# Kernel optimization log

Hardware: AMD Instinct MI355X
Metric: run time of the kernel (lower is better)

The kernel has to match this reference:

```python
import jax, jax.numpy as jnp
import numpy as np

D_MODEL = 512
EXPAND = 2
D_INNER = D_MODEL * EXPAND  # 1024
D_STATE = 64
D_CONV = 4
DT_BASE = 0.1
MAX_STEPS = 10
THRESH = 1e-4
DAMPING = 0.5
B_SZ, L = 1, 256


def setup_inputs() -> dict:
    key = jax.random.key(0)
    ks = jax.random.split(key, 12)
    rn = lambda k, shape, s=0.02: jax.random.normal(k, shape, jnp.float32) * s
    x = jax.random.normal(ks[0], (B_SZ, L, D_MODEL), jnp.float32)
    # in_proj: Linear(d_model -> 2*d_inner, bias=False); stored (in, out)
    W_in = rn(ks[1], (D_MODEL, 2 * D_INNER))
    # depthwise causal conv1d, kernel (d_inner, 1, d_conv) + bias
    conv_w = rn(ks[2], (D_INNER, 1, D_CONV), 0.2)
    conv_b = rn(ks[3], (D_INNER,), 0.02)
    # SSM kernel params (A_log initialized exactly as in the module)
    A_log = jnp.log(jnp.broadcast_to(jnp.arange(1, D_STATE + 1, dtype=jnp.float32), (D_INNER, D_STATE)))
    W_B = rn(ks[4], (D_INNER, D_STATE))
    W_C = rn(ks[5], (D_INNER, D_STATE))
    D = jnp.ones((D_INNER,), jnp.float32)
    dt_w1 = rn(ks[6], (D_INNER, D_INNER // 4))
    dt_b1 = jnp.zeros((D_INNER // 4,), jnp.float32)
    dt_w2 = rn(ks[7], (D_INNER // 4, D_INNER))
    dt_b2 = jnp.zeros((D_INNER,), jnp.float32)
    W_out = rn(ks[8], (D_INNER, D_MODEL))
    ln_in_g = jnp.ones((D_MODEL,), jnp.float32)
    ln_in_b = jnp.zeros((D_MODEL,), jnp.float32)
    ln_out_g = jnp.ones((D_MODEL,), jnp.float32)
    ln_out_b = jnp.zeros((D_MODEL,), jnp.float32)
    return dict(x=x, W_in=W_in, conv_w=conv_w, conv_b=conv_b, A_log=A_log, W_B=W_B, W_C=W_C, D=D,
                dt_w1=dt_w1, dt_b1=dt_b1, dt_w2=dt_w2, dt_b2=dt_b2, W_out=W_out,
                ln_in_g=ln_in_g, ln_in_b=ln_in_b, ln_out_g=ln_out_g, ln_out_b=ln_out_b)


def _ln(x, g, b, eps=1e-5):
    m = jnp.mean(x, axis=-1, keepdims=True)
    v = jnp.mean((x - m) ** 2, axis=-1, keepdims=True)
    return (x - m) / jnp.sqrt(v + eps) * g + b


def _forward(x, W_in, conv_w, conv_b, A_log, W_B, W_C, D, dt_w1, dt_b1, dt_w2, dt_b2, W_out,
             ln_in_g, ln_in_b, ln_out_g, ln_out_b):
    residual = x
    xn = _ln(x, ln_in_g, ln_in_b)
    xz = xn @ W_in                                  # (b, l, 2*d_inner)
    x_inner, z = jnp.split(xz, 2, axis=-1)
    # depthwise causal conv (pad d_conv-1 on the left == pad both sides then take [:L])
    xc = jnp.transpose(x_inner, (0, 2, 1))          # (b, d, l)
    xc = jax.lax.conv_general_dilated(xc, conv_w, window_strides=(1,),
                                      padding=[(D_CONV - 1, 0)],
                                      feature_group_count=D_INNER)
    xc = xc + conv_b[None, :, None]
    x_inner = jax.nn.silu(jnp.transpose(xc, (0, 2, 1)))  # (b, l, d_inner)

    # --- kernel quantities (loop-invariant: depend only on x_inner) ---
    A = -jnp.exp(A_log)                             # (d, n)
    Bm = x_inner @ W_B                              # (b, l, n)
    Cm = x_inner @ W_C                              # (b, l, n)
    dt = jax.nn.gelu(x_inner @ dt_w1 + dt_b1, approximate=False) @ dt_w2 + dt_b2
    dt = jax.nn.softplus(dt) * DT_BASE              # (b, l, d)
    A_bar = jnp.exp(jnp.einsum('bld,dn->bldn', dt, A))          # (b, l, d, n)
    Bx = (dt * x_inner)[..., None] * Bm[:, :, None, :]           # B_bar * x, (b, l, d, n)

    # --- fixed-point evolution with convergence-gated freeze (== early break) ---
    h = jnp.zeros_like(A_bar)
    y_h = h  # h_new that produces the output y
    converged = jnp.array(False)
    h_diff = jnp.float32(0.0)
    for _ in range(MAX_STEPS):
        h_new = A_bar * h + Bx
        dh = h_new - h
        diff = jnp.mean(jnp.sqrt(jnp.sum(dh * dh, axis=(-2, -1))))  # mean Frobenius norm over (b,l)
        y_h = jnp.where(converged, y_h, h_new)
        h_diff = jnp.where(converged, h_diff, diff)
        converged = converged | (diff < THRESH)
        # damping update skipped after break (converged)
        h = jnp.where(converged, h, DAMPING * h_new + (1.0 - DAMPING) * h)

    y = jnp.einsum('bldn,bln->bld', y_h, Cm) + D * x_inner
    y = y * jax.nn.silu(z)
    out = _ln(y @ W_out, ln_out_g, ln_out_b) + residual
    return out


def reference(x, W_in, conv_w, conv_b, A_log, W_B, W_C, D, dt_w1, dt_b1, dt_w2, dt_b2, W_out,
              ln_in_g, ln_in_b, ln_out_g, ln_out_b):
    return _forward(x, W_in, conv_w, conv_b, A_log, W_B, W_C, D, dt_w1, dt_b1, dt_w2, dt_b2,
                    W_out, ln_in_g, ln_in_b, ln_out_g, ln_out_b)
```

## Files before the change

kernel.cpp:

```cpp
#include <hip/hip_runtime.h>
#include <cmath>

#define L 256
#define DMODEL 512
#define DINNER 1024
#define DSTATE 64
#define NSTEPS 10

#define XZ_OFF 0
#define XI_OFF 1048576
#define BCT_OFF 1310720
#define DTB_OFF 2097152
#define ACC_OFF 3145728
#define YOP_OFF 3155968

__device__ __forceinline__ float gelu_f(float x) {
  return 0.5f * x * (1.0f + erff(x * 0.70710678118654752f));
}

__device__ __forceinline__ void mm_accum(const float (*As)[68],
                                         const float (*Bs)[64],
                                         float acc[4][4], int ty, int tx) {
#pragma unroll
  for (int kk = 0; kk < 32; ++kk) {
    const float4 av = *(const float4*)&As[kk][ty * 4];
    const float4 bv = *(const float4*)&Bs[kk][tx * 4];
    const float* ap = (const float*)&av;
    const float* bp = (const float*)&bv;
#pragma unroll
    for (int i = 0; i < 4; ++i)
#pragma unroll
      for (int j = 0; j < 4; ++j) acc[i][j] = fmaf(ap[i], bp[j], acc[i][j]);
  }
}

__device__ __forceinline__ void store_tile(float acc[4][4], float* C, int ldc,
                                           int m0, int nc, int ty, int tx) {
#pragma unroll
  for (int i = 0; i < 4; ++i)
    *(float4*)&C[(size_t)(m0 + ty * 4 + i) * ldc + nc + tx * 4] =
        *(float4*)&acc[i][0];
}

__global__ __launch_bounds__(256, 2) void k_inproj(
    const float* __restrict__ x, const float* __restrict__ g,
    const float* __restrict__ b, const float* __restrict__ W_in,
    float* __restrict__ xz) {
  __shared__ __align__(16) float As[32][68];
  __shared__ __align__(16) float Bs[32][64];
  __shared__ float pS[64][4], pQ[64][4];
  __shared__ float mrow[64], rrow[64];
  const int tid = threadIdx.x;
  const int ty = tid >> 4, tx = tid & 15;
  const int m0 = blockIdx.y * 64, n0 = blockIdx.x * 64;
  const int k0 = blockIdx.z * 256;
  {
    const int row = tid >> 2, part = tid & 3;
    const float* rp = &x[(size_t)(m0 + row) * DMODEL + part * 128];
    float s = 0.0f, q = 0.0f;
#pragma unroll
    for (int i = 0; i < 32; ++i) {
      const float4 v = *(const float4*)&rp[i * 4];
      s += v.x + v.y + v.z + v.w;
      q += v.x * v.x + v.y * v.y + v.z * v.z + v.w * v.w;
    }
    pS[row][part] = s;
    pQ[row][part] = q;
  }
  __syncthreads();
  if (tid < 64) {
    const float S = pS[tid][0] + pS[tid][1] + pS[tid][2] + pS[tid][3];
    const float Q = pQ[tid][0] + pQ[tid][1] + pQ[tid][2] + pQ[tid][3];
    const float m = S * (1.0f / DMODEL);
    const float v = Q * (1.0f / DMODEL) - m * m;
    mrow[tid] = m;
    rrow[tid] = rsqrtf(v + 1e-5f);
  }
  __syncthreads();
  float acc[4][4] = {};
  for (int t = 0; t < 8; ++t) {
    const int kb = k0 + t * 32;
#pragma unroll
    for (int i = 0; i < 2; ++i) {
      const int idx = tid + i * 256;
      const int r = idx >> 3, ck = (idx & 7) * 4;
      const float4 v = *(const float4*)&x[(size_t)(m0 + r) * DMODEL + kb + ck];
      const float* vp = (const float*)&v;
      const float m = mrow[r], rs = rrow[r];
#pragma unroll
      for (int j = 0; j < 4; ++j)
        As[ck + j][r] = (vp[j] - m) * rs * g[kb + ck + j] + b[kb + ck + j];
    }
#pragma unroll
    for (int i = 0; i < 2; ++i) {
      const int idx = tid + i * 256;
      const int r = idx >> 4, c = (idx & 15) * 4;
      *(float4*)&Bs[r][c] = *(const float4*)&W_in[(size_t)(kb + r) * 2048 + n0 + c];
    }
    __syncthreads();
    mm_accum(As, Bs, acc, ty, tx);
    __syncthreads();
  }
  store_tile(acc, xz + (size_t)blockIdx.z * 524288, 2048, m0, n0, ty, tx);
}

__global__ __launch_bounds__(256, 2) void k_bct(
    const float* __restrict__ xz, const float* __restrict__ cw,
    const float* __restrict__ cb, const float* __restrict__ W_B,
    const float* __restrict__ W_C, const float* __restrict__ W1,
    float* __restrict__ bctp, float* __restrict__ xi) {
  __shared__ __align__(16) float As[32][68];
  __shared__ __align__(16) float Bs[32][64];
  const int tid = threadIdx.x;
  const int ty = tid >> 4, tx = tid & 15;
  const int nt = blockIdx.x;
  const int m0 = blockIdx.y * 64, k0 = blockIdx.z * 128;
  const float* Bp;
  int ldb, nb;
  if (nt == 0) { Bp = W_B; ldb = 64; nb = 0; }
  else if (nt == 1) { Bp = W_C; ldb = 64; nb = 0; }
  else { Bp = W1; ldb = 256; nb = (nt - 2) * 64; }
  float acc[4][4] = {};
  for (int t = 0; t < 4; ++t) {
    const int kb = k0 + t * 32;
#pragma unroll
    for (int i = 0; i < 2; ++i) {
      const int idx = tid + i * 256;
      const int r = idx >> 3, ck = (idx & 7) * 4;
      const int l = m0 + r, d0 = kb + ck;
      float v[4];
      {
        const float4 cbv = *(const float4*)&cb[d0];
        v[0] = cbv.x; v[1] = cbv.y; v[2] = cbv.z; v[3] = cbv.w;
      }
      float4 wq[4];
#pragma unroll
      for (int j = 0; j < 4; ++j) wq[j] = *(const float4*)&cw[(d0 + j) * 4];
      const float* w0 = (const float*)&wq[0];
      const float* w1 = (const float*)&wq[1];
      const float* w2 = (const float*)&wq[2];
      const float* w3 = (const float*)&wq[3];
#pragma unroll
      for (int j = 0; j < 4; ++j) {
        const int ll = l - 3 + j;
        if (ll >= 0) {
          const float4 u0 = *(const float4*)&xz[(size_t)ll * 2048 + d0];
          const float4 u1 = *(const float4*)&xz[524288 + (size_t)ll * 2048 + d0];
          v[0] = fmaf(w0[j], u0.x + u1.x, v[0]);
          v[1] = fmaf(w1[j], u0.y + u1.y, v[1]);
          v[2] = fmaf(w2[j], u0.z + u1.z, v[2]);
          v[3] = fmaf(w3[j], u0.w + u1.w, v[3]);
        }
      }
#pragma unroll
      for (int j = 0; j < 4; ++j) v[j] = v[j] / (1.0f + expf(-v[j]));
      if (nt == 0)
        *(float4*)&xi[(size_t)l * DINNER + d0] = *(float4*)&v[0];
#pragma unroll
      for (int j = 0; j < 4; ++j) As[ck + j][r] = v[j];
    }
#pragma unroll
    for (int i = 0; i < 2; ++i) {
      const int idx = tid + i * 256;
      const int r = idx >> 4, c = (idx & 15) * 4;
      *(float4*)&Bs[r][c] = *(const float4*)&Bp[(size_t)(kb + r) * ldb + nb + c];
    }
    __syncthreads();
    mm_accum(As, Bs, acc, ty, tx);
    __syncthreads();
  }
  store_tile(acc, bctp + (size_t)blockIdx.z * 98304, 384, m0, nt * 64, ty, tx);
}

__global__ __launch_bounds__(256, 2) void k_dt2(
    const float* __restrict__ bctp, const float* __restrict__ dt_b1,
    const float* __restrict__ dt_w2, float* __restrict__ dtbp) {
  __shared__ __align__(16) float As[32][68];
  __shared__ __align__(16) float Bs[32][64];
  const int tid = threadIdx.x;
  const int ty = tid >> 4, tx = tid & 15;
  const int m0 = blockIdx.y * 64, n0 = blockIdx.x * 64;
  const int k0 = blockIdx.z * 64;
  float acc[4][4] = {};
  for (int t = 0; t < 2; ++t) {
    const int kb = k0 + t * 32;
#pragma unroll
    for (int i = 0; i < 2; ++i) {
      const int idx = tid + i * 256;
      const int r = idx >> 3, ck = (idx & 7) * 4;
      const float4 bv = *(const float4*)&dt_b1[kb + ck];
      float v[4] = {bv.x, bv.y, bv.z, bv.w};
#pragma unroll
      for (int s = 0; s < 8; ++s) {
        const float4 u =
            *(const float4*)&bctp[s * 98304 + (size_t)(m0 + r) * 384 + 128 + kb + ck];
        v[0] += u.x; v[1] += u.y; v[2] += u.z; v[3] += u.w;
      }
#pragma unroll
      for (int j = 0; j < 4; ++j) As[ck + j][r] = gelu_f(v[j]);
    }
#pragma unroll
    for (int i = 0; i < 2; ++i) {
      const int idx = tid + i * 256;
      const int r = idx >> 4, c = (idx & 15) * 4;
      *(float4*)&Bs[r][c] =
          *(const float4*)&dt_w2[(size_t)(kb + r) * 1024 + n0 + c];
    }
    __syncthreads();
    mm_accum(As, Bs, acc, ty, tx);
    __syncthreads();
  }
  store_tile(acc, dtbp + (size_t)blockIdx.z * 262144, 1024, m0, n0, ty, tx);
}

__global__ __launch_bounds__(256, 2) void k_pass1(
    const float* __restrict__ dtbp, const float* __restrict__ dt_b2,
    const float* __restrict__ xi, const float* __restrict__ bctp,
    float* __restrict__ accLp) {
  const int bx = blockIdx.x, l = blockIdx.y, tid = threadIdx.x;
  const int d = bx * 256 + tid;
  __shared__ float B2[DSTATE];
  __shared__ float sred[4][NSTEPS];
  if (tid < DSTATE) {
    float b = 0.0f;
#pragma unroll
    for (int s = 0; s < 8; ++s) b += bctp[s * 98304 + l * 384 + tid];
    B2[tid] = b * b;
  }
  __syncthreads();
  float dr = dt_b2[d];
#pragma unroll
  for (int s = 0; s < 4; ++s) dr += dtbp[s * 262144 + l * DINNER + d];
  const float sp = (dr > 20.0f) ? dr : log1pf(expf(dr));
  const float dtv = 0.1f * sp;
  const float xv = xi[l * DINNER + d];
  float w0 = dtv * xv;
  w0 *= w0;
  const float q = expf(-dtv);
  float acc[NSTEPS] = {};
  float aa = 1.0f;
  for (int n = 0; n < DSTATE; ++n) {
    aa *= q;
    const float r = fmaf(0.5f, aa, 0.5f);
    const float s2 = r * r;
    float p = w0 * B2[n];
#pragma unroll
    for (int k = 0; k < NSTEPS; ++k) {
      acc[k] += p;
      p *= s2;
    }
  }
#pragma unroll
  for (int k = 0; k < NSTEPS; ++k) {
    float v = acc[k];
#pragma unroll
    for (int off = 32; off; off >>= 1) v += __shfl_down(v, off);
    if ((tid & 63) == 0) sred[tid >> 6][k] = v;
  }
  __syncthreads();
  if (tid < NSTEPS)
    accLp[bx * (L * NSTEPS) + l * NSTEPS + tid] =
        sred[0][tid] + sred[1][tid] + sred[2][tid] + sred[3][tid];
}

__global__ __launch_bounds__(256, 2) void k_pass2(
    const float* __restrict__ dtbp, const float* __restrict__ dt_b2,
    const float* __restrict__ xi_in, const float* __restrict__ bctp,
    const float* __restrict__ xz, const float* __restrict__ Dv,
    const float* __restrict__ accLp, float* __restrict__ y) {
  const int bx = blockIdx.x, l = blockIdx.y, tid = threadIdx.x;
  const int d = bx * 256 + tid;
  __shared__ float sred[4];
  __shared__ float diffs[NSTEPS];
  __shared__ float P[DSTATE];
  __shared__ int Ksh;
#pragma unroll
  for (int k = 0; k < NSTEPS; ++k) {
    float v = 0.0f;
#pragma unroll
    for (int s = 0; s < 4; ++s) v += accLp[s * 2560 + tid * NSTEPS + k];
    v = sqrtf(v);
#pragma unroll
    for (int off = 32; off; off >>= 1) v += __shfl_down(v, off);
    if ((tid & 63) == 0) sred[tid >> 6] = v;
    __syncthreads();
    if (tid == 0)
      diffs[k] = (sred[0] + sred[1] + sred[2] + sred[3]) * (1.0f / L);
    __syncthreads();
  }
  if (tid == 0) {
    int K = NSTEPS;
    for (int k = 0; k < NSTEPS; ++k) {
      if (diffs[k] < 1e-4f) { K = k + 1; break; }
    }
    Ksh = K;
  }
  if (tid < DSTATE) {
    float bm = 0.0f, cm = 0.0f;
#pragma unroll
    for (int s = 0; s < 8; ++s) {
      bm += bctp[s * 98304 + l * 384 + tid];
      cm += bctp[s * 98304 + l * 384 + 64 + tid];
    }
    P[tid] = bm * cm;
  }
  __syncthreads();
  const int K = Ksh;
  float dr = dt_b2[d];
#pragma unroll
  for (int s = 0; s < 4; ++s) dr += dtbp[s * 262144 + l * DINNER + d];
  const float sp = (dr > 20.0f) ? dr : log1pf(expf(dr));
  const float dtv = 0.1f * sp;
  const float xv = xi_in[l * DINNER + d];
  const float dtx = dtv * xv;
  const float q = expf(-dtv);
  float aa = 1.0f, s = 0.0f;
  for (int n = 0; n < DSTATE; ++n) {
    aa *= q;
    const float r = fmaf(0.5f, aa, 0.5f);
    float c = 0.0f;
    for (int k = 1; k < K; ++k) c = fmaf(r, c, 0.5f);
    const float hn = fmaf(aa, c, 1.0f);
    s = fmaf(hn, P[n], s);
  }
  float yv = fmaf(dtx, s, Dv[d] * xv);
  const float zv = xz[l * 2048 + 1024 + d] + xz[524288 + l * 2048 + 1024 + d];
  yv *= zv / (1.0f + expf(-zv));
  y[l * DINNER + d] = yv;
}

__global__ __launch_bounds__(256, 2) void k_outproj(
    const float* __restrict__ yv, const float* __restrict__ W_out,
    float* __restrict__ yop) {
  __shared__ __align__(16) float As[32][68];
  __shared__ __align__(16) float Bs[32][64];
  const int tid = threadIdx.x;
  const int ty = tid >> 4, tx = tid & 15;
  const int m0 = blockIdx.y * 64, n0 = blockIdx.x * 64;
  const int k0 = blockIdx.z * 128;
  float acc[4][4] = {};
  for (int t = 0; t < 4; ++t) {
    const int kb = k0 + t * 32;
#pragma unroll
    for (int i = 0; i < 2; ++i) {
      const int idx = tid + i * 256;
      const int r = idx >> 3, ck = (idx & 7) * 4;
      const float4 v = *(const float4*)&yv[(size_t)(m0 + r) * DINNER + kb + ck];
      const float* vp = (const float*)&v;
#pragma unroll
      for (int j = 0; j < 4; ++j) As[ck + j][r] = vp[j];
    }
#pragma unroll
    for (int i = 0; i < 2; ++i) {
      const int idx = tid + i * 256;
      const int r = idx >> 4, c = (idx & 15) * 4;
      *(float4*)&Bs[r][c] =
          *(const float4*)&W_out[(size_t)(kb + r) * DMODEL + n0 + c];
    }
    __syncthreads();
    mm_accum(As, Bs, acc, ty, tx);
    __syncthreads();
  }
  store_tile(acc, yop + (size_t)blockIdx.z * 131072, DMODEL, m0, n0, ty, tx);
}

__global__ __launch_bounds__(256, 2) void k_ln2(
    const float* __restrict__ yop, const float* __restrict__ g,
    const float* __restrict__ b, const float* __restrict__ resid,
    float* __restrict__ out) {
  const int l = blockIdx.x, tid = threadIdx.x;
  float x0 = 0.0f, x1 = 0.0f;
#pragma unroll
  for (int s = 0; s < 8; ++s) {
    x0 += yop[s * 131072 + l * DMODEL + tid];
    x1 += yop[s * 131072 + l * DMODEL + tid + 256];
  }
  float sm = x0 + x1, q = x0 * x0 + x1 * x1;
#pragma unroll
  for (int off = 32; off; off >>= 1) {
    sm += __shfl_down(sm, off);
    q += __shfl_down(q, off);
  }
  __shared__ float sw[4], qw[4];
  __shared__ float mS, rS;
  if ((tid & 63) == 0) { sw[tid >> 6] = sm; qw[tid >> 6] = q; }
  __syncthreads();
  if (tid == 0) {
    float S = sw[0] + sw[1] + sw[2] + sw[3];
    float Q = qw[0] + qw[1] + qw[2] + qw[3];
    float m = S * (1.0f / DMODEL);
    float v = Q * (1.0f / DMODEL) - m * m;
    mS = m;
    rS = rsqrtf(v + 1e-5f);
  }
  __syncthreads();
  const float m = mS, r = rS;
  out[l * DMODEL + tid] =
      (x0 - m) * r * g[tid] + b[tid] + resid[l * DMODEL + tid];
  out[l * DMODEL + tid + 256] =
      (x1 - m) * r * g[tid + 256] + b[tid + 256] + resid[l * DMODEL + tid + 256];
}

extern "C" void kernel_launch(void* const* d_in, const int* in_sizes, int n_in,
                              void* d_out, int out_size, void* d_ws,
                              size_t ws_size, hipStream_t stream) {
  const float* x = (const float*)d_in[0];
  const float* W_in = (const float*)d_in[1];
  const float* conv_w = (const float*)d_in[2];
  const float* conv_b = (const float*)d_in[3];
  const float* W_B = (const float*)d_in[5];
  const float* W_C = (const float*)d_in[6];
  const float* Dv = (const float*)d_in[7];
  const float* dt_w1 = (const float*)d_in[8];
  const float* dt_b1 = (const float*)d_in[9];
  const float* dt_w2 = (const float*)d_in[10];
  const float* dt_b2 = (const float*)d_in[11];
  const float* W_out = (const float*)d_in[12];
  const float* ln_in_g = (const float*)d_in[13];
  const float* ln_in_b = (const float*)d_in[14];
  const float* ln_out_g = (const float*)d_in[15];
  const float* ln_out_b = (const float*)d_in[16];
  float* out = (float*)d_out;

  float* ws = (float*)d_ws;
  float* xz = ws + XZ_OFF;
  float* xi = ws + XI_OFF;
  float* bctp = ws + BCT_OFF;
  float* dtbp = ws + DTB_OFF;
  float* accLp = ws + ACC_OFF;
  float* yop = ws + YOP_OFF;

  k_inproj<<<dim3(32, 4, 2), 256, 0, stream>>>(x, ln_in_g, ln_in_b, W_in, xz);
  k_bct<<<dim3(6, 4, 8), 256, 0, stream>>>(xz, conv_w, conv_b, W_B, W_C,
                                           dt_w1, bctp, xi);
  k_dt2<<<dim3(16, 4, 4), 256, 0, stream>>>(bctp, dt_b1, dt_w2, dtbp);
  k_pass1<<<dim3(4, L), 256, 0, stream>>>(dtbp, dt_b2, xi, bctp, accLp);
  k_pass2<<<dim3(4, L), 256, 0, stream>>>(dtbp, dt_b2, xi, bctp, xz, Dv,
                                          accLp, xi);
  k_outproj<<<dim3(8, 4, 8), 256, 0, stream>>>(xi, W_out, yop);
  k_ln2<<<L, 256, 0, stream>>>(yop, ln_out_g, ln_out_b, x, out);
}
```

Before: 214.7 us.

## Split prologue work out of GEMMs into dedicated elementwise kernels

Moves LayerNorm, the causal conv plus SiLU, and the z gate out of the GEMM A-tile loaders into separate elementwise kernels (k_ln1, k_convz, k_prep). All projections then run through one generic k_gemm with different split-K factors. Precomputed B^2, B*C and the gelu'd dt hidden layer are shared by pass1 and pass2 instead of being recomputed per block. This removes redundant per-tile recomputation of conv, norm and gelu inside the GEMMs, at the cost of three extra kernel launches and extra global-memory round trips.

```diff
diff --git a/kernel.cpp b/kernel.cpp
--- a/kernel.cpp
+++ b/kernel.cpp
@@ -7,12 +7,17 @@
 #define DSTATE 64
 #define NSTEPS 10
 
-#define XZ_OFF 0
-#define XI_OFF 1048576
-#define BCT_OFF 1310720
-#define DTB_OFF 2097152
-#define ACC_OFF 3145728
-#define YOP_OFF 3155968
+#define XN_OFF 0
+#define XZ_OFF 131072
+#define XI_OFF 2228224
+#define ZS_OFF 2490368
+#define BCT_OFF 2752512
+#define T1S_OFF 3538944
+#define B2_OFF 3604480
+#define P_OFF 3620864
+#define DTB_OFF 3637248
+#define ACC_OFF 4161536
+#define YOP_OFF 4171776
 
 __device__ __forceinline__ float gelu_f(float x) {
   return 0.5f * x * (1.0f + erff(x * 0.70710678118654752f));
@@ -42,73 +47,101 @@
         *(float4*)&acc[i][0];
 }
 
-__global__ __launch_bounds__(256, 2) void k_inproj(
-    const float* __restrict__ x, const float* __restrict__ g,
-    const float* __restrict__ b, const float* __restrict__ W_in,
-    float* __restrict__ xz) {
+__global__ __launch_bounds__(256) void k_ln1(
+    const float* __restrict__ in, const float* __restrict__ g,
+    const float* __restrict__ b, float* __restrict__ out) {
+  const int l = blockIdx.x, tid = threadIdx.x;
+  const float x0 = in[l * DMODEL + tid];
+  const float x1 = in[l * DMODEL + tid + 256];
+  float sm = x0 + x1, q = x0 * x0 + x1 * x1;
+#pragma unroll
+  for (int off = 32; off; off >>= 1) {
+    sm += __shfl_down(sm, off);
+    q += __shfl_down(q, off);
+  }
+  __shared__ float sw[4], qw[4];
+  __shared__ float mS, rS;
+  if ((tid & 63) == 0) { sw[tid >> 6] = sm; qw[tid >> 6] = q; }
+  __syncthreads();
+  if (tid == 0) {
+    float S = sw[0] + sw[1] + sw[2] + sw[3];
+    float Q = qw[0] + qw[1] + qw[2] + qw[3];
+    float m = S * (1.0f / DMODEL);
+    float v = Q * (1.0f / DMODEL) - m * m;
+    mS = m;
+    rS = rsqrtf(v + 1e-5f);
+  }
+  __syncthreads();
+  out[l * DMODEL + tid] = (x0 - mS) * rS * g[tid] + b[tid];
+  out[l * DMODEL + tid + 256] = (x1 - mS) * rS * g[tid + 256] + b[tid + 256];
+}
+
+__global__ __launch_bounds__(256, 2) void k_gemm(
+    const float* __restrict__ A, int lda, const float* __restrict__ B, int ldb,
+    float* __restrict__ C, int ldc, int cslice, int kchunk) {
   __shared__ __align__(16) float As[32][68];
   __shared__ __align__(16) float Bs[32][64];
-  __shared__ float pS[64][4], pQ[64][4];
-  __shared__ float mrow[64], rrow[64];
   const int tid = threadIdx.x;
   const int ty = tid >> 4, tx = tid & 15;
   const int m0 = blockIdx.y * 64, n0 = blockIdx.x * 64;
-  const int k0 = blockIdx.z * 256;
-  {
-    const int row = tid >> 2, part = tid & 3;
-    const float* rp = &x[(size_t)(m0 + row) * DMODEL + part * 128];
-    float s = 0.0f, q = 0.0f;
-#pragma unroll
-    for (int i = 0; i < 32; ++i) {
-      const float4 v = *(const float4*)&rp[i * 4];
-      s += v.x + v.y + v.z + v.w;
-      q += v.x * v.x + v.y * v.y + v.z * v.z + v.w * v.w;
-    }
-    pS[row][part] = s;
-    pQ[row][part] = q;
-  }
-  __syncthreads();
-  if (tid < 64) {
-    const float S = pS[tid][0] + pS[tid][1] + pS[tid][2] + pS[tid][3];
-    const float Q = pQ[tid][0] + pQ[tid][1] + pQ[tid][2] + pQ[tid][3];
-    const float m = S * (1.0f / DMODEL);
-    const float v = Q * (1.0f / DMODEL) - m * m;
-    mrow[tid] = m;
-    rrow[tid] = rsqrtf(v + 1e-5f);
-  }
-  __syncthreads();
+  const int k0 = blockIdx.z * kchunk;
+  const int ktiles = kchunk >> 5;
   float acc[4][4] = {};
-  for (int t = 0; t < 8; ++t) {
+  for (int t = 0; t < ktiles; ++t) {
     const int kb = k0 + t * 32;
 #pragma unroll
     for (int i = 0; i < 2; ++i) {
       const int idx = tid + i * 256;
       const int r = idx >> 3, ck = (idx & 7) * 4;
-      const float4 v = *(const float4*)&x[(size_t)(m0 + r) * DMODEL + kb + ck];
-      const float* vp = (const float*)&v;
-      const float m = mrow[r], rs = rrow[r];
-#pragma unroll
-      for (int j = 0; j < 4; ++j)
-        As[ck + j][r] = (vp[j] - m) * rs * g[kb + ck + j] + b[kb + ck + j];
+      const float4 v = *(const float4*)&A[(size_t)(m0 + r) * lda + kb + ck];
+      As[ck + 0][r] = v.x;
+      As[ck + 1][r] = v.y;
+      As[ck + 2][r] = v.z;
+      As[ck + 3][r] = v.w;
     }
 #pragma unroll
     for (int i = 0; i < 2; ++i) {
       const int idx = tid + i * 256;
       const int r = idx >> 4, c = (idx & 15) * 4;
-      *(float4*)&Bs[r][c] = *(const float4*)&W_in[(size_t)(kb + r) * 2048 + n0 + c];
+      *(float4*)&Bs[r][c] = *(const float4*)&B[(size_t)(kb + r) * ldb + n0 + c];
     }
     __syncthreads();
     mm_accum(As, Bs, acc, ty, tx);
     __syncthreads();
   }
-  store_tile(acc, xz + (size_t)blockIdx.z * 524288, 2048, m0, n0, ty, tx);
+  store_tile(acc, C + (size_t)blockIdx.z * cslice, ldc, m0, n0, ty, tx);
+}
+
+__global__ __launch_bounds__(256) void k_convz(
+    const float* __restrict__ xz, const float* __restrict__ cw,
+    const float* __restrict__ cb, float* __restrict__ xi,
+    float* __restrict__ zs) {
+  const int d = blockIdx.x * 256 + threadIdx.x;
+  const int l = blockIdx.y;
+  const float4 w = *(const float4*)&cw[d * 4];
+  const float* wp = (const float*)&w;
+  float s = cb[d];
+#pragma unroll
+  for (int j = 0; j < 4; ++j) {
+    const int ll = l - 3 + j;
+    if (ll >= 0) {
+      float u = 0.0f;
+#pragma unroll
+      for (int sl = 0; sl < 4; ++sl) u += xz[sl * 524288 + ll * 2048 + d];
+      s = fmaf(wp[j], u, s);
+    }
+  }
+  xi[l * DINNER + d] = s / (1.0f + expf(-s));
+  float z = 0.0f;
+#pragma unroll
+  for (int sl = 0; sl < 4; ++sl) z += xz[sl * 524288 + l * 2048 + 1024 + d];
+  zs[l * DINNER + d] = z / (1.0f + expf(-z));
 }
 
 __global__ __launch_bounds__(256, 2) void k_bct(
-    const float* __restrict__ xz, const float* __restrict__ cw,
-    const float* __restrict__ cb, const float* __restrict__ W_B,
+    const float* __restrict__ xi, const float* __restrict__ W_B,
     const float* __restrict__ W_C, const float* __restrict__ W1,
-    float* __restrict__ bctp, float* __restrict__ xi) {
+    float* __restrict__ bctp) {
   __shared__ __align__(16) float As[32][68];
   __shared__ __align__(16) float Bs[32][64];
   const int tid = threadIdx.x;
@@ -127,37 +160,11 @@
     for (int i = 0; i < 2; ++i) {
       const int idx = tid + i * 256;
       const int r = idx >> 3, ck = (idx & 7) * 4;
-      const int l = m0 + r, d0 = kb + ck;
-      float v[4];
-      {
-        const float4 cbv = *(const float4*)&cb[d0];
-        v[0] = cbv.x; v[1] = cbv.y; v[2] = cbv.z; v[3] = cbv.w;
-      }
-      float4 wq[4];
-#pragma unroll
-      for (int j = 0; j < 4; ++j) wq[j] = *(const float4*)&cw[(d0 + j) * 4];
-      const float* w0 = (const float*)&wq[0];
-      const float* w1 = (const float*)&wq[1];
-      const float* w2 = (const float*)&wq[2];
-      const float* w3 = (const float*)&wq[3];
-#pragma unroll
-      for (int j = 0; j < 4; ++j) {
-        const int ll = l - 3 + j;
-        if (ll >= 0) {
-          const float4 u0 = *(const float4*)&xz[(size_t)ll * 2048 + d0];
-          const float4 u1 = *(const float4*)&xz[524288 + (size_t)ll * 2048 + d0];
-          v[0] = fmaf(w0[j], u0.x + u1.x, v[0]);
-          v[1] = fmaf(w1[j], u0.y + u1.y, v[1]);
-          v[2] = fmaf(w2[j], u0.z + u1.z, v[2]);
-          v[3] = fmaf(w3[j], u0.w + u1.w, v[3]);
-        }
-      }
-#pragma unroll
-      for (int j = 0; j < 4; ++j) v[j] = v[j] / (1.0f + expf(-v[j]));
-      if (nt == 0)
-        *(float4*)&xi[(size_t)l * DINNER + d0] = *(float4*)&v[0];
-#pragma unroll
-      for (int j = 0; j < 4; ++j) As[ck + j][r] = v[j];
+      const float4 v = *(const float4*)&xi[(size_t)(m0 + r) * DINNER + kb + ck];
+      As[ck + 0][r] = v.x;
+      As[ck + 1][r] = v.y;
+      As[ck + 2][r] = v.z;
+      As[ck + 3][r] = v.w;
     }
 #pragma unroll
     for (int i = 0; i < 2; ++i) {
@@ -172,65 +179,38 @@
   store_tile(acc, bctp + (size_t)blockIdx.z * 98304, 384, m0, nt * 64, ty, tx);
 }
 
-__global__ __launch_bounds__(256, 2) void k_dt2(
+__global__ __launch_bounds__(256) void k_prep(
     const float* __restrict__ bctp, const float* __restrict__ dt_b1,
-    const float* __restrict__ dt_w2, float* __restrict__ dtbp) {
-  __shared__ __align__(16) float As[32][68];
-  __shared__ __align__(16) float Bs[32][64];
-  const int tid = threadIdx.x;
-  const int ty = tid >> 4, tx = tid & 15;
-  const int m0 = blockIdx.y * 64, n0 = blockIdx.x * 64;
-  const int k0 = blockIdx.z * 64;
-  float acc[4][4] = {};
-  for (int t = 0; t < 2; ++t) {
-    const int kb = k0 + t * 32;
-#pragma unroll
-    for (int i = 0; i < 2; ++i) {
-      const int idx = tid + i * 256;
-      const int r = idx >> 3, ck = (idx & 7) * 4;
-      const float4 bv = *(const float4*)&dt_b1[kb + ck];
-      float v[4] = {bv.x, bv.y, bv.z, bv.w};
-#pragma unroll
-      for (int s = 0; s < 8; ++s) {
-        const float4 u =
-            *(const float4*)&bctp[s * 98304 + (size_t)(m0 + r) * 384 + 128 + kb + ck];
-        v[0] += u.x; v[1] += u.y; v[2] += u.z; v[3] += u.w;
-      }
-#pragma unroll
-      for (int j = 0; j < 4; ++j) As[ck + j][r] = gelu_f(v[j]);
-    }
-#pragma unroll
-    for (int i = 0; i < 2; ++i) {
-      const int idx = tid + i * 256;
-      const int r = idx >> 4, c = (idx & 15) * 4;
-      *(float4*)&Bs[r][c] =
-          *(const float4*)&dt_w2[(size_t)(kb + r) * 1024 + n0 + c];
-    }
-    __syncthreads();
-    mm_accum(As, Bs, acc, ty, tx);
-    __syncthreads();
-  }
-  store_tile(acc, dtbp + (size_t)blockIdx.z * 262144, 1024, m0, n0, ty, tx);
-}
-
-__global__ __launch_bounds__(256, 2) void k_pass1(
+    float* __restrict__ t1s, float* __restrict__ B2, float* __restrict__ P) {
+  const int l = blockIdx.x, c = threadIdx.x;
+  float t = dt_b1[c];
+#pragma unroll
+  for (int s = 0; s < 8; ++s) t += bctp[s * 98304 + l * 384 + 128 + c];
+  t1s[l * 256 + c] = gelu_f(t);
+  if (c < DSTATE) {
+    float b = 0.0f, cc = 0.0f;
+#pragma unroll
+    for (int s = 0; s < 8; ++s) {
+      b += bctp[s * 98304 + l * 384 + c];
+      cc += bctp[s * 98304 + l * 384 + 64 + c];
+    }
+    B2[l * 64 + c] = b * b;
+    P[l * 64 + c] = b * cc;
+  }
+}
+
+__global__ __launch_bounds__(256) void k_pass1(
     const float* __restrict__ dtbp, const float* __restrict__ dt_b2,
-    const float* __restrict__ xi, const float* __restrict__ bctp,
+    const float* __restrict__ xi, const float* __restrict__ B2g,
     float* __restrict__ accLp) {
   const int bx = blockIdx.x, l = blockIdx.y, tid = threadIdx.x;
   const int d = bx * 256 + tid;
   __shared__ float B2[DSTATE];
   __shared__ float sred[4][NSTEPS];
-  if (tid < DSTATE) {
-    float b = 0.0f;
-#pragma unroll
-    for (int s = 0; s < 8; ++s) b += bctp[s * 98304 + l * 384 + tid];
-    B2[tid] = b * b;
-  }
-  __syncthreads();
-  float dr = dt_b2[d];
-#pragma unroll
-  for (int s = 0; s < 4; ++s) dr += dtbp[s * 262144 + l * DINNER + d];
+  if (tid < DSTATE) B2[tid] = B2g[l * 64 + tid];
+  __syncthreads();
+  const float dr =
+      dt_b2[d] + dtbp[l * DINNER + d] + dtbp[262144 + l * DINNER + d];
   const float sp = (dr > 20.0f) ? dr : log1pf(expf(dr));
   const float dtv = 0.1f * sp;
   const float xv = xi[l * DINNER + d];
@@ -263,10 +243,10 @@
         sred[0][tid] + sred[1][tid] + sred[2][tid] + sred[3][tid];
 }
 
-__global__ __launch_bounds__(256, 2) void k_pass2(
+__global__ __launch_bounds__(256) void k_pass2(
     const float* __restrict__ dtbp, const float* __restrict__ dt_b2,
-    const float* __restrict__ xi_in, const float* __restrict__ bctp,
-    const float* __restrict__ xz, const float* __restrict__ Dv,
+    const float* __restrict__ xi_in, const float* __restrict__ Pg,
+    const float* __restrict__ zs, const float* __restrict__ Dv,
     const float* __restrict__ accLp, float* __restrict__ y) {
   const int bx = blockIdx.x, l = blockIdx.y, tid = threadIdx.x;
   const int d = bx * 256 + tid;
@@ -295,20 +275,11 @@
     }
     Ksh = K;
   }
-  if (tid < DSTATE) {
-    float bm = 0.0f, cm = 0.0f;
-#pragma unroll
-    for (int s = 0; s < 8; ++s) {
-      bm += bctp[s * 98304 + l * 384 + tid];
-      cm += bctp[s * 98304 + l * 384 + 64 + tid];
-    }
-    P[tid] = bm * cm;
-  }
+  if (tid < DSTATE) P[tid] = Pg[l * 64 + tid];
   __syncthreads();
   const int K = Ksh;
-  float dr = dt_b2[d];
-#pragma unroll
-  for (int s = 0; s < 4; ++s) dr += dtbp[s * 262144 + l * DINNER + d];
+  const float dr =
+      dt_b2[d] + dtbp[l * DINNER + d] + dtbp[262144 + l * DINNER + d];
   const float sp = (dr > 20.0f) ? dr : log1pf(expf(dr));
   const float dtv = 0.1f * sp;
   const float xv = xi_in[l * DINNER + d];
@@ -324,47 +295,11 @@
     s = fmaf(hn, P[n], s);
   }
   float yv = fmaf(dtx, s, Dv[d] * xv);
-  const float zv = xz[l * 2048 + 1024 + d] + xz[524288 + l * 2048 + 1024 + d];
-  yv *= zv / (1.0f + expf(-zv));
+  yv *= zs[l * DINNER + d];
   y[l * DINNER + d] = yv;
 }
 
-__global__ __launch_bounds__(256, 2) void k_outproj(
-    const float* __restrict__ yv, const float* __restrict__ W_out,
-    float* __restrict__ yop) {
-  __shared__ __align__(16) float As[32][68];
-  __shared__ __align__(16) float Bs[32][64];
-  const int tid = threadIdx.x;
-  const int ty = tid >> 4, tx = tid & 15;
-  const int m0 = blockIdx.y * 64, n0 = blockIdx.x * 64;
-  const int k0 = blockIdx.z * 128;
-  float acc[4][4] = {};
-  for (int t = 0; t < 4; ++t) {
-    const int kb = k0 + t * 32;
-#pragma unroll
-    for (int i = 0; i < 2; ++i) {
-      const int idx = tid + i * 256;
-      const int r = idx >> 3, ck = (idx & 7) * 4;
-      const float4 v = *(const float4*)&yv[(size_t)(m0 + r) * DINNER + kb + ck];
-      const float* vp = (const float*)&v;
-#pragma unroll
-      for (int j = 0; j < 4; ++j) As[ck + j][r] = vp[j];
-    }
-#pragma unroll
-    for (int i = 0; i < 2; ++i) {
-      const int idx = tid + i * 256;
-      const int r = idx >> 4, c = (idx & 15) * 4;
-      *(float4*)&Bs[r][c] =
-          *(const float4*)&W_out[(size_t)(kb + r) * DMODEL + n0 + c];
-    }
-    __syncthreads();
-    mm_accum(As, Bs, acc, ty, tx);
-    __syncthreads();
-  }
-  store_tile(acc, yop + (size_t)blockIdx.z * 131072, DMODEL, m0, n0, ty, tx);
-}
-
-__global__ __launch_bounds__(256, 2) void k_ln2(
+__global__ __launch_bounds__(256) void k_ln2(
     const float* __restrict__ yop, const float* __restrict__ g,
     const float* __restrict__ b, const float* __restrict__ resid,
     float* __restrict__ out) {
@@ -394,11 +329,10 @@
     rS = rsqrtf(v + 1e-5f);
   }
   __syncthreads();
-  const float m = mS, r = rS;
   out[l * DMODEL + tid] =
-      (x0 - m) * r * g[tid] + b[tid] + resid[l * DMODEL + tid];
-  out[l * DMODEL + tid + 256] =
-      (x1 - m) * r * g[tid + 256] + b[tid + 256] + resid[l * DMODEL + tid + 256];
+      (x0 - mS) * rS * g[tid] + b[tid] + resid[l * DMODEL + tid];
+  out[l * DMODEL + tid + 256] = (x1 - mS) * rS * g[tid + 256] + b[tid + 256] +
+                                resid[l * DMODEL + tid + 256];
 }
 
 extern "C" void kernel_launch(void* const* d_in, const int* in_sizes, int n_in,
@@ -423,20 +357,30 @@
   float* out = (float*)d_out;
 
   float* ws = (float*)d_ws;
+  float* xn = ws + XN_OFF;
   float* xz = ws + XZ_OFF;
   float* xi = ws + XI_OFF;
+  float* zs = ws + ZS_OFF;
   float* bctp = ws + BCT_OFF;
+  float* t1s = ws + T1S_OFF;
+  float* B2 = ws + B2_OFF;
+  float* P = ws + P_OFF;
   float* dtbp = ws + DTB_OFF;
   float* accLp = ws + ACC_OFF;
   float* yop = ws + YOP_OFF;
 
-  k_inproj<<<dim3(32, 4, 2), 256, 0, stream>>>(x, ln_in_g, ln_in_b, W_in, xz);
-  k_bct<<<dim3(6, 4, 8), 256, 0, stream>>>(xz, conv_w, conv_b, W_B, W_C,
-                                           dt_w1, bctp, xi);
-  k_dt2<<<dim3(16, 4, 4), 256, 0, stream>>>(bctp, dt_b1, dt_w2, dtbp);
-  k_pass1<<<dim3(4, L), 256, 0, stream>>>(dtbp, dt_b2, xi, bctp, accLp);
-  k_pass2<<<dim3(4, L), 256, 0, stream>>>(dtbp, dt_b2, xi, bctp, xz, Dv,
-                                          accLp, xi);
-  k_outproj<<<dim3(8, 4, 8), 256, 0, stream>>>(xi, W_out, yop);
+  k_ln1<<<L, 256, 0, stream>>>(x, ln_in_g, ln_in_b, xn);
+  k_gemm<<<dim3(32, 4, 4), 256, 0, stream>>>(xn, DMODEL, W_in, 2048, xz, 2048,
+                                             524288, 128);
+  k_convz<<<dim3(4, L), 256, 0, stream>>>(xz, conv_w, conv_b, xi, zs);
+  k_bct<<<dim3(6, 4, 8), 256, 0, stream>>>(xi, W_B, W_C, dt_w1, bctp);
+  k_prep<<<L, 256, 0, stream>>>(bctp, dt_b1, t1s, B2, P);
+  k_gemm<<<dim3(16, 4, 2), 256, 0, stream>>>(t1s, 256, dt_w2, 1024, dtbp, 1024,
+                                             262144, 128);
+  k_pass1<<<dim3(4, L), 256, 0, stream>>>(dtbp, dt_b2, xi, B2, accLp);
+  k_pass2<<<dim3(4, L), 256, 0, stream>>>(dtbp, dt_b2, xi, P, zs, Dv, accLp,
+                                          xi);
+  k_gemm<<<dim3(8, 4, 8), 256, 0, stream>>>(xi, DINNER, W_out, DMODEL, yop,
+                                            DMODEL, 131072, 128);
   k_ln2<<<L, 256, 0, stream>>>(yop, ln_out_g, ln_out_b, x, out);
 }
```

After: 180.8 us. -15.8%, faster.
